# Kernel tuning notes

Measured on AMD Instinct MI355X. Metric: run time of the kernel, lower is better.

Reference implementation:

```python
import jax, jax.numpy as jnp
import numpy as np
import math

N_NODES = 50000
N_EDGES = 800000
HIDDEN = 128
NUM_GAUSS = 50
NUM_FILTERS = 128
CUTOFF = 10.0
SHIFT = math.log(2.0)


def setup_inputs() -> dict:
    key = jax.random.key(0)
    ks = jax.random.split(key, 12)
    x = jax.random.normal(ks[0], (N_NODES, HIDDEN), dtype=jnp.float32)
    edge_index = jax.random.randint(ks[1], (2, N_EDGES), 0, N_NODES, dtype=jnp.int64)
    edge_weight = jax.random.uniform(ks[2], (N_EDGES,), dtype=jnp.float32)
    edge_attr = jax.random.normal(ks[3], (N_EDGES, NUM_GAUSS), dtype=jnp.float32)
    # learned parameters (xavier-ish scale)
    def xavier(k, shape):
        fan_in, fan_out = shape[1], shape[0]
        bound = math.sqrt(6.0 / (fan_in + fan_out))
        return jax.random.uniform(k, shape, dtype=jnp.float32, minval=-bound, maxval=bound)
    mlp_w1 = xavier(ks[4], (NUM_FILTERS, NUM_GAUSS))
    mlp_b1 = jnp.zeros((NUM_FILTERS,), jnp.float32)
    mlp_w2 = xavier(ks[5], (NUM_FILTERS, NUM_FILTERS))
    mlp_b2 = jnp.zeros((NUM_FILTERS,), jnp.float32)
    lin1_w = xavier(ks[6], (NUM_FILTERS, HIDDEN))   # no bias
    lin2_w = xavier(ks[7], (HIDDEN, NUM_FILTERS))
    lin2_b = jnp.zeros((HIDDEN,), jnp.float32)
    lin_w = xavier(ks[8], (HIDDEN, HIDDEN))
    lin_b = jnp.zeros((HIDDEN,), jnp.float32)
    return {"x": x, "edge_index": edge_index, "edge_weight": edge_weight,
            "edge_attr": edge_attr, "mlp_w1": mlp_w1, "mlp_b1": mlp_b1,
            "mlp_w2": mlp_w2, "mlp_b2": mlp_b2, "lin1_w": lin1_w,
            "lin2_w": lin2_w, "lin2_b": lin2_b, "lin_w": lin_w, "lin_b": lin_b}


def shifted_softplus(v):
    return jax.nn.softplus(v) - SHIFT


def reference(x, edge_index, edge_weight, edge_attr, mlp_w1, mlp_b1,
              mlp_w2, mlp_b2, lin1_w, lin2_w, lin2_b, lin_w, lin_b):
    src, dst = edge_index[0], edge_index[1]
    # cosine cutoff per edge: [E]
    C = 0.5 * (jnp.cos(edge_weight * (jnp.pi / CUTOFF)) + 1.0)
    # edge filter MLP: [E, num_filters]
    h_e = shifted_softplus(edge_attr @ mlp_w1.T + mlp_b1)
    W = (h_e @ mlp_w2.T + mlp_b2) * C[:, None]
    # node projection, gather-multiply-scatter aggregation
    h = x @ lin1_w.T                       # [N, num_filters]
    msg = h[src] * W                       # [E, num_filters]
    agg = jax.ops.segment_sum(msg, dst, num_segments=N_NODES)  # [N, num_filters]
    h = agg @ lin2_w.T + lin2_b            # [N, hidden]
    h = shifted_softplus(h)
    out = h @ lin_w.T + lin_b              # [N, hidden]
    return out
```

## Files before the change

kernel.cpp:

```cpp
#include <hip/hip_runtime.h>
#include <hip/hip_bf16.h>
#include <math.h>

#define E_NUM 800000
#define NN 50000
#define NG 50
#define NTW (E_NUM / 16)
#define EDGE_BLOCKS 512

typedef __bf16 bf16x8 __attribute__((ext_vector_type(8)));
typedef float f32x4 __attribute__((ext_vector_type(4)));
typedef unsigned short ushortx8 __attribute__((ext_vector_type(8)));

__device__ __forceinline__ unsigned short f2b(float f) {
  union { __bf16 h; unsigned short u; } v; v.h = (__bf16)f; return v.u;
}
__device__ __forceinline__ float b2f(unsigned short u) {
  union { unsigned u; float f; } v; v.u = ((unsigned)u) << 16; return v.f;
}
__device__ __forceinline__ float sspf(float v) {
  float e = __builtin_amdgcn_exp2f(-1.4426950408889634f * fabsf(v));
  return fmaxf(v, 0.f) + 0.6931471805599453f * __builtin_amdgcn_logf(fmaf(0.5f, e, 0.5f));
}

__global__ __launch_bounds__(256) void k_hist(const int* __restrict__ ei, int* __restrict__ counts) {
  int e = blockIdx.x * 256 + threadIdx.x;
  if (e < E_NUM) atomicAdd(&counts[ei[E_NUM + e]], 1);
}

__global__ __launch_bounds__(1024) void k_scan(const int* __restrict__ counts,
                                               int* __restrict__ cursor) {
  __shared__ int tot[1024];
  const int t = threadIdx.x;
  const int C = (NN + 1023) >> 10;
  int lo = t * C, hi = lo + C; if (hi > NN) hi = NN; if (lo > NN) lo = NN;
  int s = 0;
  for (int i = lo; i < hi; ++i) s += counts[i];
  tot[t] = s;
  __syncthreads();
  int mine = s;
  for (int o = 1; o < 1024; o <<= 1) {
    int v = (t >= o) ? tot[t - o] : 0;
    __syncthreads();
    tot[t] += v;
    __syncthreads();
  }
  int run = tot[t] - mine;
  for (int i = lo; i < hi; ++i) { int c = counts[i]; cursor[i] = run; run += c; }
}

__global__ __launch_bounds__(256) void k_scatter2(
    const int* __restrict__ ei, const float* __restrict__ ew,
    const float* __restrict__ attr, int* __restrict__ cursor,
    int* __restrict__ srcS, int* __restrict__ dstS,
    float* __restrict__ cS, unsigned short* __restrict__ attrS)
{
  int e = blockIdx.x * 256 + threadIdx.x;
  if (e >= E_NUM) return;
  int d = ei[E_NUM + e];
  int pos = atomicAdd(&cursor[d], 1);
  srcS[pos] = ei[e];
  dstS[pos] = d;
  cS[pos] = 0.5f * (__builtin_amdgcn_cosf(ew[e] * 0.05f) + 1.f);
  const float* rp = attr + (long)e * NG;
  unsigned short* op = attrS + (long)pos * 64;
  float2 v[25];
#pragma unroll
  for (int i = 0; i < 25; ++i) v[i] = *(const float2*)(rp + 2 * i);
#pragma unroll
  for (int c = 0; c < 8; ++c) {
    ushortx8 o;
#pragma unroll
    for (int j = 0; j < 8; ++j) {
      int k = c * 8 + j;
      o[j] = (k < NG) ? f2b((k & 1) ? v[k >> 1].y : v[k >> 1].x) : (unsigned short)0;
    }
    *(ushortx8*)(op + c * 8) = o;
  }
}

__global__ __launch_bounds__(256) void k_mfma_gemm(
    const float* __restrict__ X, const float* __restrict__ Wm,
    const float* __restrict__ bias, float* __restrict__ out, int act, int nrows)
{
  __shared__ __attribute__((aligned(16))) unsigned short s_x[128 * 128];
  __shared__ __attribute__((aligned(16))) unsigned short s_w[128 * 128];
  const int tid = threadIdx.x;
  const int w = tid >> 6, lane = tid & 63, q = lane >> 4, n16 = lane & 15;
  const int base = blockIdx.x * 128;

  for (int c = tid; c < 128 * 16; c += 256) {
    int f = c >> 4, ch = c & 15;
    const float4* wp = (const float4*)(Wm + f * 128 + ch * 8);
    float4 v0 = wp[0], v1 = wp[1];
    ushortx8 v = { f2b(v0.x), f2b(v0.y), f2b(v0.z), f2b(v0.w),
                   f2b(v1.x), f2b(v1.y), f2b(v1.z), f2b(v1.w) };
    *(ushortx8*)&s_w[(f << 7) + ((ch ^ (f & 15)) << 3)] = v;
  }
  for (int c = tid; c < 128 * 16; c += 256) {
    int r = c >> 4, ch = c & 15;
    int n = base + r;
    float4 v0 = {0.f, 0.f, 0.f, 0.f}, v1 = v0;
    if (n < nrows) {
      const float4* xp = (const float4*)(X + (long)n * 128 + ch * 8);
      v0 = xp[0]; v1 = xp[1];
    }
    ushortx8 v = { f2b(v0.x), f2b(v0.y), f2b(v0.z), f2b(v0.w),
                   f2b(v1.x), f2b(v1.y), f2b(v1.z), f2b(v1.w) };
    *(ushortx8*)&s_x[(r << 7) + ((ch ^ (r & 15)) << 3)] = v;
  }
  __syncthreads();

  float bv[8];
#pragma unroll
  for (int t = 0; t < 8; ++t) bv[t] = bias ? bias[t * 16 + n16] : 0.f;

  bf16x8 a[2][4];
#pragma unroll
  for (int g = 0; g < 2; ++g) {
    int r = w * 32 + g * 16 + n16;
#pragma unroll
    for (int ks = 0; ks < 4; ++ks)
      a[g][ks] = *(const bf16x8*)&s_x[(r << 7) + (((ks * 4 + q) ^ (r & 15)) << 3)];
  }
#pragma unroll
  for (int t = 0; t < 8; ++t) {
    int f = t * 16 + n16;
    bf16x8 b[4];
#pragma unroll
    for (int ks = 0; ks < 4; ++ks)
      b[ks] = *(const bf16x8*)&s_w[(f << 7) + (((ks * 4 + q) ^ (f & 15)) << 3)];
#pragma unroll
    for (int g = 0; g < 2; ++g) {
      f32x4 acc = {0.f, 0.f, 0.f, 0.f};
#pragma unroll
      for (int ks = 0; ks < 4; ++ks)
        acc = __builtin_amdgcn_mfma_f32_16x16x32_bf16(a[g][ks], b[ks], acc, 0, 0, 0);
#pragma unroll
      for (int r = 0; r < 4; ++r) {
        int n = base + w * 32 + g * 16 + q * 4 + r;
        if (n < nrows) {
          float v = acc[r] + bv[t];
          if (act) v = sspf(v);
          out[(long)n * 128 + f] = v;
        }
      }
    }
  }
}

__global__ __launch_bounds__(256, 2) void k_gemm23(
    const float* __restrict__ A, const float* __restrict__ W2,
    const float* __restrict__ B2, const float* __restrict__ W3,
    const float* __restrict__ B3, float* __restrict__ out, int nrows)
{
  __shared__ __attribute__((aligned(16))) unsigned short s_x[128 * 128];
  __shared__ __attribute__((aligned(16))) unsigned short s_w[128 * 128];
  const int tid = threadIdx.x;
  const int w = tid >> 6, lane = tid & 63, q = lane >> 4, n16 = lane & 15;
  const int base = blockIdx.x * 128;

  for (int c = tid; c < 128 * 16; c += 256) {
    int f = c >> 4, ch = c & 15;
    const float4* wp = (const float4*)(W2 + f * 128 + ch * 8);
    float4 v0 = wp[0], v1 = wp[1];
    ushortx8 v = { f2b(v0.x), f2b(v0.y), f2b(v0.z), f2b(v0.w),
                   f2b(v1.x), f2b(v1.y), f2b(v1.z), f2b(v1.w) };
    *(ushortx8*)&s_w[(f << 7) + ((ch ^ (f & 15)) << 3)] = v;
  }
  for (int c = tid; c < 128 * 16; c += 256) {
    int r = c >> 4, ch = c & 15;
    int n = base + r;
    float4 v0 = {0.f, 0.f, 0.f, 0.f}, v1 = v0;
    if (n < nrows) {
      const float4* xp = (const float4*)(A + (long)n * 128 + ch * 8);
      v0 = xp[0]; v1 = xp[1];
    }
    ushortx8 v = { f2b(v0.x), f2b(v0.y), f2b(v0.z), f2b(v0.w),
                   f2b(v1.x), f2b(v1.y), f2b(v1.z), f2b(v1.w) };
    *(ushortx8*)&s_x[(r << 7) + ((ch ^ (r & 15)) << 3)] = v;
  }
  __syncthreads();

  float b2v[8], b3v[8];
#pragma unroll
  for (int t = 0; t < 8; ++t) { b2v[t] = B2[t * 16 + n16]; b3v[t] = B3[t * 16 + n16]; }

  bf16x8 a[2][4];
#pragma unroll
  for (int g = 0; g < 2; ++g) {
    int r = w * 32 + g * 16 + n16;
#pragma unroll
    for (int ks = 0; ks < 4; ++ks)
      a[g][ks] = *(const bf16x8*)&s_x[(r << 7) + (((ks * 4 + q) ^ (r & 15)) << 3)];
  }
  float acc1[8][2][4];
#pragma unroll
  for (int t = 0; t < 8; ++t) {
    int f = t * 16 + n16;
    bf16x8 b[4];
#pragma unroll
    for (int ks = 0; ks < 4; ++ks)
      b[ks] = *(const bf16x8*)&s_w[(f << 7) + (((ks * 4 + q) ^ (f & 15)) << 3)];
#pragma unroll
    for (int g = 0; g < 2; ++g) {
      f32x4 acc = {0.f, 0.f, 0.f, 0.f};
#pragma unroll
      for (int ks = 0; ks < 4; ++ks)
        acc = __builtin_amdgcn_mfma_f32_16x16x32_bf16(a[g][ks], b[ks], acc, 0, 0, 0);
#pragma unroll
      for (int r = 0; r < 4; ++r) acc1[t][g][r] = acc[r];
    }
  }
  __syncthreads();

#pragma unroll
  for (int t = 0; t < 8; ++t) {
    int f = t * 16 + n16;
#pragma unroll
    for (int g = 0; g < 2; ++g)
#pragma unroll
      for (int r = 0; r < 4; ++r) {
        int row = w * 32 + g * 16 + q * 4 + r;
        s_x[(row << 7) + (((f >> 3) ^ (row & 15)) << 3) + (f & 7)] =
            f2b(sspf(acc1[t][g][r] + b2v[t]));
      }
  }
  for (int c = tid; c < 128 * 16; c += 256) {
    int f = c >> 4, ch = c & 15;
    const float4* wp = (const float4*)(W3 + f * 128 + ch * 8);
    float4 v0 = wp[0], v1 = wp[1];
    ushortx8 v = { f2b(v0.x), f2b(v0.y), f2b(v0.z), f2b(v0.w),
                   f2b(v1.x), f2b(v1.y), f2b(v1.z), f2b(v1.w) };
    *(ushortx8*)&s_w[(f << 7) + ((ch ^ (f & 15)) << 3)] = v;
  }
  __syncthreads();

#pragma unroll
  for (int g = 0; g < 2; ++g) {
    int r = w * 32 + g * 16 + n16;
#pragma unroll
    for (int ks = 0; ks < 4; ++ks)
      a[g][ks] = *(const bf16x8*)&s_x[(r << 7) + (((ks * 4 + q) ^ (r & 15)) << 3)];
  }
#pragma unroll
  for (int t = 0; t < 8; ++t) {
    int f = t * 16 + n16;
    bf16x8 b[4];
#pragma unroll
    for (int ks = 0; ks < 4; ++ks)
      b[ks] = *(const bf16x8*)&s_w[(f << 7) + (((ks * 4 + q) ^ (f & 15)) << 3)];
#pragma unroll
    for (int g = 0; g < 2; ++g) {
      f32x4 acc = {0.f, 0.f, 0.f, 0.f};
#pragma unroll
      for (int ks = 0; ks < 4; ++ks)
        acc = __builtin_amdgcn_mfma_f32_16x16x32_bf16(a[g][ks], b[ks], acc, 0, 0, 0);
#pragma unroll
      for (int r = 0; r < 4; ++r) {
        int n = base + w * 32 + g * 16 + q * 4 + r;
        if (n < nrows) out[(long)n * 128 + f] = acc[r] + b3v[t];
      }
    }
  }
}

__global__ __launch_bounds__(512, 4) void k_edge_agg(
    const float* __restrict__ attr, const int* __restrict__ ei,
    const float* __restrict__ ew, const float* __restrict__ w1,
    const float* __restrict__ b1, const float* __restrict__ w2,
    const float* __restrict__ b2, const float* __restrict__ h,
    const int* __restrict__ srcS, const int* __restrict__ dstS,
    const float* __restrict__ cS, const unsigned short* __restrict__ attrS,
    float* __restrict__ agg, int mode)
{
  __shared__ __attribute__((aligned(16))) unsigned short s_w2[128 * 128];
  __shared__ __attribute__((aligned(16))) unsigned short s_scr[8 * 16 * 136];

  const int tid  = threadIdx.x;
  const int w    = tid >> 6;
  const int lane = tid & 63;
  const int q    = lane >> 4;
  const int n16  = lane & 15;

  for (int i = tid; i < 128 * 128; i += 512) {
    int f = i >> 7, k = i & 127;
    int pos = (f << 7) + ((((k >> 3) ^ (f & 15)) << 3)) + (k & 7);
    s_w2[pos] = f2b(w2[i]);
  }
  bf16x8 w1A[8], w1B[8];
#pragma unroll
  for (int t = 0; t < 8; ++t) {
    int f = t * 16 + n16;
    const float* row = w1 + f * NG;
    union { ushortx8 u; bf16x8 b; } ua, ub;
#pragma unroll
    for (int j = 0; j < 8; ++j) ua.u[j] = f2b(row[q * 8 + j]);
#pragma unroll
    for (int j = 0; j < 8; ++j) { int k = 32 + q * 8 + j; ub.u[j] = (k < NG) ? f2b(row[k]) : (unsigned short)0; }
    w1A[t] = ua.b; w1B[t] = ub.b;
  }
  float b1v[8], b2v[8];
#pragma unroll
  for (int t = 0; t < 8; ++t) {
    b1v[t] = b1[t * 16 + n16];
    b2v[t] = b2[t * 16 + n16];
  }
  __syncthreads();

  unsigned short* scr = s_scr + w * (16 * 136);
  const int nwaves = EDGE_BLOCKS * 8;
  const int gw = blockIdx.x * 8 + w;

  if (mode == 1) {
    bf16x8 uaN, ubN;
    {
      const long e0 = (long)gw * 16;
      uaN = *(const bf16x8*)(attrS + (e0 + n16) * 64 + q * 8);
      ubN = *(const bf16x8*)(attrS + (e0 + n16) * 64 + 32 + q * 8);
    }

    for (int tile = gw; tile < NTW; tile += nwaves) {
      const int e0 = tile * 16;
      bf16x8 uaC = uaN, ubC = ubN;

#pragma unroll
      for (int t = 0; t < 8; ++t) {
        f32x4 acc = {0.f, 0.f, 0.f, 0.f};
        acc = __builtin_amdgcn_mfma_f32_16x16x32_bf16(uaC, w1A[t], acc, 0, 0, 0);
        acc = __builtin_amdgcn_mfma_f32_16x16x32_bf16(ubC, w1B[t], acc, 0, 0, 0);
        int f = t * 16 + n16;
#pragma unroll
        for (int r = 0; r < 4; ++r) {
          int row = q * 4 + r;
          scr[row * 136 + f] = f2b(sspf(acc[r] + b1v[t]));
        }
      }
      __builtin_amdgcn_wave_barrier();

      bf16x8 a2f[4];
#pragma unroll
      for (int ks = 0; ks < 4; ++ks)
        a2f[ks] = *(const bf16x8*)&scr[n16 * 136 + ks * 32 + q * 8];
      __builtin_amdgcn_wave_barrier();

      {
        const int tn = tile + nwaves;
        if (tn < NTW) {
          const long en = (long)tn * 16;
          uaN = *(const bf16x8*)(attrS + (en + n16) * 64 + q * 8);
          ubN = *(const bf16x8*)(attrS + (en + n16) * 64 + 32 + q * 8);
        }
      }

      float cvv[4];
#pragma unroll
      for (int r = 0; r < 4; ++r) cvv[r] = cS[e0 + q * 4 + r];

#pragma unroll
      for (int t = 0; t < 8; ++t) {
        int f = t * 16 + n16;
        f32x4 acc = {0.f, 0.f, 0.f, 0.f};
#pragma unroll
        for (int ks = 0; ks < 4; ++ks) {
          bf16x8 bb = *(const bf16x8*)&s_w2[(f << 7) + (((ks * 4 + q) ^ (f & 15)) << 3)];
          acc = __builtin_amdgcn_mfma_f32_16x16x32_bf16(a2f[ks], bb, acc, 0, 0, 0);
        }
#pragma unroll
        for (int r = 0; r < 4; ++r) {
          int row = q * 4 + r;
          scr[row * 136 + f] = f2b((acc[r] + b2v[t]) * cvv[r]);
        }
      }
      __builtin_amdgcn_wave_barrier();

      int dcur = -1, rowstart = 0;
      float ax = 0.f, ay = 0.f;
#pragma unroll
      for (int hf = 0; hf < 2; ++hf) {
        int dv[8]; float2 hv[8];
#pragma unroll
        for (int i = 0; i < 8; ++i) {
          int pos = e0 + hf * 8 + i;
          dv[i] = __builtin_amdgcn_readfirstlane(dstS[pos]);
          int sv = __builtin_amdgcn_readfirstlane(srcS[pos]);
          hv[i] = *(const float2*)(h + (long)sv * 128 + (lane << 1));
        }
#pragma unroll
        for (int i = 0; i < 8; ++i) {
          int row = hf * 8 + i;
          if (dv[i] != dcur) {
            if (dcur >= 0) {
              float* ap = agg + (long)dcur * 128 + (lane << 1);
              if (rowstart == 0) { atomicAdd(ap, ax); atomicAdd(ap + 1, ay); }
              else { float2 o; o.x = ax; o.y = ay; *(float2*)ap = o; }
            }
            dcur = dv[i]; ax = 0.f; ay = 0.f; rowstart = row;
          }
          unsigned wp = *(const unsigned*)&scr[row * 136 + (lane << 1)];
          ax = fmaf(hv[i].x, b2f((unsigned short)(wp & 0xffffu)), ax);
          ay = fmaf(hv[i].y, b2f((unsigned short)(wp >> 16)), ay);
        }
      }
      {
        float* ap = agg + (long)dcur * 128 + (lane << 1);
        atomicAdd(ap, ax); atomicAdd(ap + 1, ay);
      }
      __builtin_amdgcn_wave_barrier();
    }
  } else {
    for (int tile = gw; tile < NTW; tile += nwaves) {
      const int e0 = tile * 16;
      const int er = e0 + n16;
      const float* rp = attr + (long)er * NG;

      float2 p0 = *(const float2*)(rp + q * 8);
      float2 p1 = *(const float2*)(rp + q * 8 + 2);
      float2 p2 = *(const float2*)(rp + q * 8 + 4);
      float2 p3 = *(const float2*)(rp + q * 8 + 6);
      float2 p4 = {0.f, 0.f}, p5 = {0.f, 0.f}, p6 = {0.f, 0.f}, p7 = {0.f, 0.f};
      if (q < 2) {
        const float* rp2 = rp + 32 + q * 8;
        p4 = *(const float2*)(rp2);
        p5 = *(const float2*)(rp2 + 2);
        p6 = *(const float2*)(rp2 + 4);
        p7 = *(const float2*)(rp2 + 6);
      } else if (q == 2) {
        p4 = *(const float2*)(rp + 48);
      }
      union { ushortx8 u; bf16x8 b; } ua, ub;
      ua.u[0] = f2b(p0.x); ua.u[1] = f2b(p0.y); ua.u[2] = f2b(p1.x); ua.u[3] = f2b(p1.y);
      ua.u[4] = f2b(p2.x); ua.u[5] = f2b(p2.y); ua.u[6] = f2b(p3.x); ua.u[7] = f2b(p3.y);
      ub.u[0] = f2b(p4.x); ub.u[1] = f2b(p4.y); ub.u[2] = f2b(p5.x); ub.u[3] = f2b(p5.y);
      ub.u[4] = f2b(p6.x); ub.u[5] = f2b(p6.y); ub.u[6] = f2b(p7.x); ub.u[7] = f2b(p7.y);

#pragma unroll
      for (int t = 0; t < 8; ++t) {
        f32x4 acc = {0.f, 0.f, 0.f, 0.f};
        acc = __builtin_amdgcn_mfma_f32_16x16x32_bf16(ua.b, w1A[t], acc, 0, 0, 0);
        acc = __builtin_amdgcn_mfma_f32_16x16x32_bf16(ub.b, w1B[t], acc, 0, 0, 0);
        int f = t * 16 + n16;
#pragma unroll
        for (int r = 0; r < 4; ++r) {
          int row = q * 4 + r;
          scr[row * 136 + f] = f2b(sspf(acc[r] + b1v[t]));
        }
      }
      __builtin_amdgcn_wave_barrier();

      bf16x8 a2f[4];
#pragma unroll
      for (int ks = 0; ks < 4; ++ks)
        a2f[ks] = *(const bf16x8*)&scr[n16 * 136 + ks * 32 + q * 8];
      __builtin_amdgcn_wave_barrier();

      float cvv[4];
      int srcv[4], dstv[4];
#pragma unroll
      for (int r = 0; r < 4; ++r) {
        cvv[r] = 0.5f * (__builtin_amdgcn_cosf(ew[e0 + q * 4 + r] * 0.05f) + 1.f);
        srcv[r] = ei[e0 + q * 4 + r];
        dstv[r] = ei[E_NUM + e0 + q * 4 + r];
      }

#pragma unroll
      for (int t = 0; t < 8; ++t) {
        int f = t * 16 + n16;
        f32x4 acc = {0.f, 0.f, 0.f, 0.f};
#pragma unroll
        for (int ks = 0; ks < 4; ++ks) {
          bf16x8 bb = *(const bf16x8*)&s_w2[(f << 7) + (((ks * 4 + q) ^ (f & 15)) << 3)];
          acc = __builtin_amdgcn_mfma_f32_16x16x32_bf16(a2f[ks], bb, acc, 0, 0, 0);
        }
#pragma unroll
        for (int r = 0; r < 4; ++r) {
          float msg = h[(long)srcv[r] * 128 + f] * (acc[r] + b2v[t]) * cvv[r];
          atomicAdd(&agg[(long)dstv[r] * 128 + f], msg);
        }
      }
      __builtin_amdgcn_wave_barrier();
    }
  }
}

extern "C" void kernel_launch(void* const* d_in, const int* in_sizes, int n_in,
                              void* d_out, int out_size, void* d_ws, size_t ws_size,
                              hipStream_t stream) {
  const float* x     = (const float*)d_in[0];
  const int*   ei    = (const int*)  d_in[1];
  const float* ew    = (const float*)d_in[2];
  const float* attr  = (const float*)d_in[3];
  const float* w1    = (const float*)d_in[4];
  const float* b1    = (const float*)d_in[5];
  const float* w2    = (const float*)d_in[6];
  const float* b2    = (const float*)d_in[7];
  const float* lin1w = (const float*)d_in[8];
  const float* lin2w = (const float*)d_in[9];
  const float* lin2b = (const float*)d_in[10];
  const float* linw  = (const float*)d_in[11];
  const float* linb  = (const float*)d_in[12];
  float* out = (float*)d_out;

  char* base = (char*)d_ws;
  float* agg    = (float*)base;
  float* h      = agg + (size_t)NN * 128;
  int*   counts = (int*)(h + (size_t)NN * 128);
  int*   cursor = counts + NN;
  int*   srcS   = cursor + NN;
  int*   dstS   = srcS + E_NUM;
  float* cS     = (float*)(dstS + E_NUM);
  size_t head   = (size_t)((char*)(cS + E_NUM) - base);
  size_t aoff   = (head + 255) & ~(size_t)255;
  unsigned short* attrS = (unsigned short*)(base + aoff);
  size_t need   = aoff + (size_t)E_NUM * 64 * sizeof(unsigned short);
  const int mode = (ws_size >= need) ? 1 : 0;

  const int gemm_grid = (NN + 127) / 128;
  (void)hipMemsetAsync(agg, 0, (size_t)NN * 128 * sizeof(float), stream);
  if (mode == 1) {
    (void)hipMemsetAsync(counts, 0, (size_t)NN * sizeof(int), stream);
    k_hist<<<(E_NUM + 255) / 256, 256, 0, stream>>>(ei, counts);
    k_scan<<<1, 1024, 0, stream>>>(counts, cursor);
    k_scatter2<<<(E_NUM + 255) / 256, 256, 0, stream>>>(ei, ew, attr, cursor,
                                                        srcS, dstS, cS, attrS);
  }
  k_mfma_gemm<<<gemm_grid, 256, 0, stream>>>(x, lin1w, nullptr, h, 0, NN);
  k_edge_agg<<<EDGE_BLOCKS, 512, 0, stream>>>(attr, ei, ew, w1, b1, w2, b2, h,
                                              srcS, dstS, cS, attrS, agg, mode);
  k_gemm23<<<gemm_grid, 256, 0, stream>>>(agg, lin2w, lin2b, linw, linb, out, NN);
}
```

Before: 611.5 us.

## Gather edge attributes through a sorted index instead of materialising permuted bf16 copy

The scatter kernel now stores only the original edge index per sorted position, not a permuted bf16 copy of the 50-wide edge attributes. The edge aggregation kernel gathers fp32 attribute rows through that index, converting to bf16 on the fly and prefetching the next tile's index and row. This removes one full read and write pass over the attribute array, at the cost of non-contiguous reads of 200-byte rows and an extra level of indirection in the hot loop.

```diff
diff --git a/kernel.cpp b/kernel.cpp
--- a/kernel.cpp
+++ b/kernel.cpp
@@ -21,6 +21,31 @@
 __device__ __forceinline__ float sspf(float v) {
   float e = __builtin_amdgcn_exp2f(-1.4426950408889634f * fabsf(v));
   return fmaxf(v, 0.f) + 0.6931471805599453f * __builtin_amdgcn_logf(fmaf(0.5f, e, 0.5f));
+}
+
+__device__ __forceinline__ void gather_attr(const float* __restrict__ attr, int idx, int q,
+                                            bf16x8& ua, bf16x8& ub) {
+  const float* rp = attr + (long)idx * NG;
+  float2 p0 = *(const float2*)(rp + q * 8);
+  float2 p1 = *(const float2*)(rp + q * 8 + 2);
+  float2 p2 = *(const float2*)(rp + q * 8 + 4);
+  float2 p3 = *(const float2*)(rp + q * 8 + 6);
+  float2 p4 = {0.f, 0.f}, p5 = {0.f, 0.f}, p6 = {0.f, 0.f}, p7 = {0.f, 0.f};
+  if (q < 2) {
+    const float* rp2 = rp + 32 + q * 8;
+    p4 = *(const float2*)(rp2);
+    p5 = *(const float2*)(rp2 + 2);
+    p6 = *(const float2*)(rp2 + 4);
+    p7 = *(const float2*)(rp2 + 6);
+  } else if (q == 2) {
+    p4 = *(const float2*)(rp + 48);
+  }
+  union { ushortx8 u; bf16x8 b; } a, bb;
+  a.u[0] = f2b(p0.x); a.u[1] = f2b(p0.y); a.u[2] = f2b(p1.x); a.u[3] = f2b(p1.y);
+  a.u[4] = f2b(p2.x); a.u[5] = f2b(p2.y); a.u[6] = f2b(p3.x); a.u[7] = f2b(p3.y);
+  bb.u[0] = f2b(p4.x); bb.u[1] = f2b(p4.y); bb.u[2] = f2b(p5.x); bb.u[3] = f2b(p5.y);
+  bb.u[4] = f2b(p6.x); bb.u[5] = f2b(p6.y); bb.u[6] = f2b(p7.x); bb.u[7] = f2b(p7.y);
+  ua = a.b; ub = bb.b;
 }
 
 __global__ __launch_bounds__(256) void k_hist(const int* __restrict__ ei, int* __restrict__ counts) {
@@ -51,9 +76,8 @@
 
 __global__ __launch_bounds__(256) void k_scatter2(
     const int* __restrict__ ei, const float* __restrict__ ew,
-    const float* __restrict__ attr, int* __restrict__ cursor,
-    int* __restrict__ srcS, int* __restrict__ dstS,
-    float* __restrict__ cS, unsigned short* __restrict__ attrS)
+    int* __restrict__ cursor, int* __restrict__ srcS, int* __restrict__ dstS,
+    float* __restrict__ cS, int* __restrict__ eS)
 {
   int e = blockIdx.x * 256 + threadIdx.x;
   if (e >= E_NUM) return;
@@ -62,21 +86,7 @@
   srcS[pos] = ei[e];
   dstS[pos] = d;
   cS[pos] = 0.5f * (__builtin_amdgcn_cosf(ew[e] * 0.05f) + 1.f);
-  const float* rp = attr + (long)e * NG;
-  unsigned short* op = attrS + (long)pos * 64;
-  float2 v[25];
-#pragma unroll
-  for (int i = 0; i < 25; ++i) v[i] = *(const float2*)(rp + 2 * i);
-#pragma unroll
-  for (int c = 0; c < 8; ++c) {
-    ushortx8 o;
-#pragma unroll
-    for (int j = 0; j < 8; ++j) {
-      int k = c * 8 + j;
-      o[j] = (k < NG) ? f2b((k & 1) ? v[k >> 1].y : v[k >> 1].x) : (unsigned short)0;
-    }
-    *(ushortx8*)(op + c * 8) = o;
-  }
+  eS[pos] = e;
 }
 
 __global__ __launch_bounds__(256) void k_mfma_gemm(
@@ -271,7 +281,7 @@
     const float* __restrict__ b1, const float* __restrict__ w2,
     const float* __restrict__ b2, const float* __restrict__ h,
     const int* __restrict__ srcS, const int* __restrict__ dstS,
-    const float* __restrict__ cS, const unsigned short* __restrict__ attrS,
+    const float* __restrict__ cS, const int* __restrict__ eS,
     float* __restrict__ agg, int mode)
 {
   __shared__ __attribute__((aligned(16))) unsigned short s_w2[128 * 128];
@@ -313,16 +323,17 @@
   const int gw = blockIdx.x * 8 + w;
 
   if (mode == 1) {
-    bf16x8 uaN, ubN;
-    {
-      const long e0 = (long)gw * 16;
-      uaN = *(const bf16x8*)(attrS + (e0 + n16) * 64 + q * 8);
-      ubN = *(const bf16x8*)(attrS + (e0 + n16) * 64 + 32 + q * 8);
+    bf16x8 uaN = {}, ubN = {};
+    int idxN = 0;
+    if (gw < NTW) {
+      int idx0 = eS[(long)gw * 16 + n16];
+      gather_attr(attr, idx0, q, uaN, ubN);
+      if (gw + nwaves < NTW) idxN = eS[(long)(gw + nwaves) * 16 + n16];
     }
 
     for (int tile = gw; tile < NTW; tile += nwaves) {
       const int e0 = tile * 16;
-      bf16x8 uaC = uaN, ubC = ubN;
+      const bf16x8 uaC = uaN, ubC = ubN;
 
 #pragma unroll
       for (int t = 0; t < 8; ++t) {
@@ -344,14 +355,9 @@
         a2f[ks] = *(const bf16x8*)&scr[n16 * 136 + ks * 32 + q * 8];
       __builtin_amdgcn_wave_barrier();
 
-      {
-        const int tn = tile + nwaves;
-        if (tn < NTW) {
-          const long en = (long)tn * 16;
-          uaN = *(const bf16x8*)(attrS + (en + n16) * 64 + q * 8);
-          ubN = *(const bf16x8*)(attrS + (en + n16) * 64 + 32 + q * 8);
-        }
-      }
+      const int tn = tile + nwaves;
+      if (tn < NTW) gather_attr(attr, idxN, q, uaN, ubN);
+      if (tn + nwaves < NTW) idxN = eS[(long)(tn + nwaves) * 16 + n16];
 
       float cvv[4];
 #pragma unroll
@@ -411,34 +417,14 @@
   } else {
     for (int tile = gw; tile < NTW; tile += nwaves) {
       const int e0 = tile * 16;
-      const int er = e0 + n16;
-      const float* rp = attr + (long)er * NG;
-
-      float2 p0 = *(const float2*)(rp + q * 8);
-      float2 p1 = *(const float2*)(rp + q * 8 + 2);
-      float2 p2 = *(const float2*)(rp + q * 8 + 4);
-      float2 p3 = *(const float2*)(rp + q * 8 + 6);
-      float2 p4 = {0.f, 0.f}, p5 = {0.f, 0.f}, p6 = {0.f, 0.f}, p7 = {0.f, 0.f};
-      if (q < 2) {
-        const float* rp2 = rp + 32 + q * 8;
-        p4 = *(const float2*)(rp2);
-        p5 = *(const float2*)(rp2 + 2);
-        p6 = *(const float2*)(rp2 + 4);
-        p7 = *(const float2*)(rp2 + 6);
-      } else if (q == 2) {
-        p4 = *(const float2*)(rp + 48);
-      }
-      union { ushortx8 u; bf16x8 b; } ua, ub;
-      ua.u[0] = f2b(p0.x); ua.u[1] = f2b(p0.y); ua.u[2] = f2b(p1.x); ua.u[3] = f2b(p1.y);
-      ua.u[4] = f2b(p2.x); ua.u[5] = f2b(p2.y); ua.u[6] = f2b(p3.x); ua.u[7] = f2b(p3.y);
-      ub.u[0] = f2b(p4.x); ub.u[1] = f2b(p4.y); ub.u[2] = f2b(p5.x); ub.u[3] = f2b(p5.y);
-      ub.u[4] = f2b(p6.x); ub.u[5] = f2b(p6.y); ub.u[6] = f2b(p7.x); ub.u[7] = f2b(p7.y);
+      bf16x8 ua, ub;
+      gather_attr(attr, e0 + n16, q, ua, ub);
 
 #pragma unroll
       for (int t = 0; t < 8; ++t) {
         f32x4 acc = {0.f, 0.f, 0.f, 0.f};
-        acc = __builtin_amdgcn_mfma_f32_16x16x32_bf16(ua.b, w1A[t], acc, 0, 0, 0);
-        acc = __builtin_amdgcn_mfma_f32_16x16x32_bf16(ub.b, w1B[t], acc, 0, 0, 0);
+        acc = __builtin_amdgcn_mfma_f32_16x16x32_bf16(ua, w1A[t], acc, 0, 0, 0);
+        acc = __builtin_amdgcn_mfma_f32_16x16x32_bf16(ub, w1B[t], acc, 0, 0, 0);
         int f = t * 16 + n16;
 #pragma unroll
         for (int r = 0; r < 4; ++r) {
@@ -509,10 +495,8 @@
   int*   srcS   = cursor + NN;
   int*   dstS   = srcS + E_NUM;
   float* cS     = (float*)(dstS + E_NUM);
-  size_t head   = (size_t)((char*)(cS + E_NUM) - base);
-  size_t aoff   = (head + 255) & ~(size_t)255;
-  unsigned short* attrS = (unsigned short*)(base + aoff);
-  size_t need   = aoff + (size_t)E_NUM * 64 * sizeof(unsigned short);
+  int*   eS     = (int*)(cS + E_NUM);
+  size_t need   = (size_t)((char*)(eS + E_NUM) - base);
   const int mode = (ws_size >= need) ? 1 : 0;
 
   const int gemm_grid = (NN + 127) / 128;
@@ -521,11 +505,10 @@
     (void)hipMemsetAsync(counts, 0, (size_t)NN * sizeof(int), stream);
     k_hist<<<(E_NUM + 255) / 256, 256, 0, stream>>>(ei, counts);
     k_scan<<<1, 1024, 0, stream>>>(counts, cursor);
-    k_scatter2<<<(E_NUM + 255) / 256, 256, 0, stream>>>(ei, ew, attr, cursor,
-                                                        srcS, dstS, cS, attrS);
+    k_scatter2<<<(E_NUM + 255) / 256, 256, 0, stream>>>(ei, ew, cursor, srcS, dstS, cS, eS);
   }
   k_mfma_gemm<<<gemm_grid, 256, 0, stream>>>(x, lin1w, nullptr, h, 0, NN);
   k_edge_agg<<<EDGE_BLOCKS, 512, 0, stream>>>(attr, ei, ew, w1, b1, w2, b2, h,
-                                              srcS, dstS, cS, attrS, agg, mode);
+                                              srcS, dstS, cS, eS, agg, mode);
   k_gemm23<<<gemm_grid, 256, 0, stream>>>(agg, lin2w, lin2b, linw, linb, out, NN);
 }
```

Measured after the change: 618.9 us. Within noise of the previous version (+1.2%).
